# Performance work log

Measured on AMD Instinct MI355X. Metric: run time of the kernel, lower is better.

Reference implementation:

```python
import jax, jax.numpy as jnp
import numpy as np

N = 50000      # nodes
E = 800000     # edges
DIN = 256
DH = 256
DOUT = 64


def setup_inputs() -> dict:
    key = jax.random.key(0)
    ks = jax.random.split(key, 8)
    x = jax.random.normal(ks[0], (N, DIN), dtype=jnp.float32)
    edge_index = jax.random.randint(ks[1], (2, E), 0, N, dtype=jnp.int64)
    s = 0.05
    W1 = jax.random.normal(ks[2], (DIN, DH), dtype=jnp.float32) * s
    b1 = jnp.zeros((DH,), dtype=jnp.float32)
    W2 = jax.random.normal(ks[3], (DH, DH), dtype=jnp.float32) * s
    b2 = jnp.zeros((DH,), dtype=jnp.float32)
    W3 = jax.random.normal(ks[4], (DH, DOUT), dtype=jnp.float32) * s
    b3 = jnp.zeros((DOUT,), dtype=jnp.float32)
    return {"x": x, "edge_index": edge_index, "W1": W1, "b1": b1,
            "W2": W2, "b2": b2, "W3": W3, "b3": b3}


def gcn_conv(x, src, dst, deg_inv_sqrt, W, b):
    # x: [N, din] -> [N, dout]. PyG GCNConv: h = D^{-1/2}(A+I)D^{-1/2} (x W) + b
    n = x.shape[0]
    h = x @ W                                   # [N, dout]
    norm = deg_inv_sqrt[src] * deg_inv_sqrt[dst]  # [E+N]
    msgs = h[src] * norm[:, None]               # gather + scale, [E+N, dout]
    out = jax.ops.segment_sum(msgs, dst, num_segments=n)  # scatter-add
    return out + b


def _loops(edge_index, n):
    # add self loops, compute symmetric normalization degrees
    sl = jnp.arange(n, dtype=edge_index.dtype)
    src = jnp.concatenate([edge_index[0], sl])
    dst = jnp.concatenate([edge_index[1], sl])
    deg = jax.ops.segment_sum(jnp.ones_like(dst, dtype=jnp.float32), dst, num_segments=n)
    dis = jnp.where(deg > 0, jax.lax.rsqrt(deg), 0.0)
    return src, dst, dis


def reference(x, edge_index, W1, b1, W2, b2, W3, b3):
    src, dst, dis = _loops(edge_index, x.shape[0])
    h = jax.nn.relu(gcn_conv(x, src, dst, dis, W1, b1))   # dropout: eval no-op
    h = jax.nn.relu(gcn_conv(h, src, dst, dis, W2, b2))
    out = gcn_conv(h, src, dst, dis, W3, b3)              # batch=None -> no pooling
    return out
```

## Files before the change

kernel.cpp:

```cpp
#include <hip/hip_runtime.h>
#include <hip/hip_fp8.h>
#include <cstdint>
#include <cstddef>

typedef unsigned short u16;
typedef _Float16 f16x8 __attribute__((ext_vector_type(8)));
typedef float f32x2 __attribute__((ext_vector_type(2)));
typedef float f32x4 __attribute__((ext_vector_type(4)));

#if defined(__has_builtin)
#if __has_builtin(__builtin_amdgcn_cvt_pk_f32_fp8) && __has_builtin(__builtin_amdgcn_cvt_pk_fp8_f32)
#define FP8_BUILTIN 1
#endif
#endif

__device__ __forceinline__ float h2f(u16 u) {
  return (float)__builtin_bit_cast(_Float16, u);
}
__device__ __forceinline__ u16 f2h(float f) {
  return __builtin_bit_cast(u16, (_Float16)f);
}
__device__ __forceinline__ unsigned char ftofp8(float f) {
#ifdef FP8_BUILTIN
  return (unsigned char)(__builtin_amdgcn_cvt_pk_fp8_f32(f, f, 0, false) & 0xFF);
#else
  return __hip_fp8_e4m3(f).__x;
#endif
}

__device__ __forceinline__ void async16(u16* lds, const u16* g) {
  __builtin_amdgcn_global_load_lds(
      (const __attribute__((address_space(1))) unsigned int*)g,
      (__attribute__((address_space(3))) unsigned int*)lds, 16, 0, 0);
}

__device__ __forceinline__ void fma8(float* a, float d, uint4 p) {
  a[0] += d * h2f((u16)p.x); a[1] += d * h2f((u16)(p.x >> 16));
  a[2] += d * h2f((u16)p.y); a[3] += d * h2f((u16)(p.y >> 16));
  a[4] += d * h2f((u16)p.z); a[5] += d * h2f((u16)(p.z >> 16));
  a[6] += d * h2f((u16)p.w); a[7] += d * h2f((u16)(p.w >> 16));
}

__device__ __forceinline__ void fma8p(float* a, float d, uint2 p) {
#ifdef FP8_BUILTIN
  f32x2 v0 = __builtin_amdgcn_cvt_pk_f32_fp8((int)p.x, false);
  f32x2 v1 = __builtin_amdgcn_cvt_pk_f32_fp8((int)p.x, true);
  f32x2 v2 = __builtin_amdgcn_cvt_pk_f32_fp8((int)p.y, false);
  f32x2 v3 = __builtin_amdgcn_cvt_pk_f32_fp8((int)p.y, true);
  a[0] += d * v0.x; a[1] += d * v0.y; a[2] += d * v1.x; a[3] += d * v1.y;
  a[4] += d * v2.x; a[5] += d * v2.y; a[6] += d * v3.x; a[7] += d * v3.y;
#else
  const unsigned char* b = (const unsigned char*)&p;
#pragma unroll
  for (int k = 0; k < 8; ++k) {
    __hip_fp8_e4m3 v; v.__x = b[k];
    a[k] += d * (float)v;
  }
#endif
}

__device__ __forceinline__ int wave_is64(const void* ep) {
  const unsigned* p = (const unsigned*)ep;
  const int lane = threadIdx.x & 63;
  unsigned v = p[2 * lane + 1] | p[2 * (lane + 64) + 1];
  unsigned long long bal = __ballot(v != 0u);
  return (bal == 0ull) ? 1 : 0;
}

__device__ __forceinline__ int edge_at(const void* ep, int is64, long long idx) {
  if (is64) return (int)((const long long*)ep)[idx];
  return ((const int*)ep)[idx];
}

#define NCHUNK 64

__global__ void zero_f32(float* p, int n) {
  int i = blockIdx.x * 256 + threadIdx.x;
  if (i < n) p[i] = 0.f;
}

__global__ __launch_bounds__(256) void prep_all(
    const float4* __restrict__ x, ushort4* __restrict__ xpad, int n_src4, int n_tot4,
    const float* __restrict__ W1, u16* __restrict__ wt1,
    const float* __restrict__ W2, u16* __restrict__ wt2,
    const float* __restrict__ W3, u16* __restrict__ wt3,
    const void* __restrict__ ep, int* __restrict__ cnt,
    int E, int N, int DIN, int DH, int DOUT,
    int nb_cvt, int nb_w1, int nb_w2, int nb_w3) {
  int b = blockIdx.x;
  if (b < nb_cvt) {
    int i = b * 256 + threadIdx.x;
    if (i < n_tot4) {
      ushort4 o = {0, 0, 0, 0};
      if (i < n_src4) {
        float4 v = x[i];
        o.x = f2h(v.x); o.y = f2h(v.y); o.z = f2h(v.z); o.w = f2h(v.w);
      }
      xpad[i] = o;
    }
    return;
  }
  b -= nb_cvt;
  if (b < nb_w1) {
    int idx = b * 256 + threadIdx.x;
    if (idx < DIN * DH) {
      int n = idx / DIN, k = idx % DIN;
      wt1[idx] = f2h(W1[k * DH + n]);
    }
    return;
  }
  b -= nb_w1;
  if (b < nb_w2) {
    int idx = b * 256 + threadIdx.x;
    if (idx < DH * DH) {
      int n = idx / DH, k = idx % DH;
      wt2[idx] = f2h(W2[k * DH + n]);
    }
    return;
  }
  b -= nb_w2;
  if (b < nb_w3) {
    int idx = b * 256 + threadIdx.x;
    if (idx < DH * DOUT) {
      int n = idx / DH, k = idx % DH;
      wt3[idx] = f2h(W3[k * DOUT + n]);
    }
    return;
  }
  b -= nb_w3;
  {
    __shared__ int h[256];
    h[threadIdx.x] = 0;
    __syncthreads();
    int is64 = wave_is64(ep);
    const int per = (E + NCHUNK - 1) / NCHUNK;
    const int e0 = b * per, e1 = min(e0 + per, E);
    for (int e = e0 + (int)threadIdx.x; e < e1; e += 256) {
      int d = edge_at(ep, is64, (long long)E + e);
      d = min(max(d, 0), N - 1);
      atomicAdd(&h[d >> 8], 1);
    }
    __syncthreads();
    cnt[threadIdx.x * NCHUNK + b] = h[threadIdx.x];
  }
}

__global__ __launch_bounds__(256) void csr_base(const int* __restrict__ cnt,
                                                int* __restrict__ bases,
                                                int* __restrict__ off,
                                                int nbuck, int E) {
  __shared__ int ws4[8];
  const int t = threadIdx.x, lane = t & 63, w = t >> 6;
  int tot = 0;
  if (t < nbuck)
#pragma unroll 8
    for (int c = 0; c < NCHUNK; ++c) tot += cnt[t * NCHUNK + c];
  int inc = tot;
#pragma unroll
  for (int o = 1; o < 64; o <<= 1) {
    int u = __shfl_up(inc, o, 64);
    if (lane >= o) inc += u;
  }
  if (lane == 63) ws4[w] = inc;
  __syncthreads();
  if (t == 0) {
    int run = 0;
#pragma unroll
    for (int k = 0; k < 4; ++k) { int v = ws4[k]; ws4[k + 4] = run; run += v; }
  }
  __syncthreads();
  const int base = ws4[w + 4] + inc - tot;
  if (t < nbuck) {
    bases[t] = base;
    int run = base;
    for (int c = 0; c < NCHUNK; ++c) {
      off[t * NCHUNK + c] = run;
      run += cnt[t * NCHUNK + c];
    }
  }
  if (t == 0) bases[nbuck] = E;
}

__global__ __launch_bounds__(256) void csr_bucket(const void* __restrict__ ep,
                                                  const int* __restrict__ off,
                                                  unsigned* __restrict__ tmp,
                                                  int E, int N) {
  __shared__ int cur[256];
  const int chunk = blockIdx.x;
  const int nbuck = (N + 255) >> 8;
  if ((int)threadIdx.x < nbuck) cur[threadIdx.x] = off[threadIdx.x * NCHUNK + chunk];
  __syncthreads();
  int is64 = wave_is64(ep);
  const int per = (E + NCHUNK - 1) / NCHUNK;
  const int e0 = chunk * per, e1 = min(e0 + per, E);
  for (int e = e0 + (int)threadIdx.x; e < e1; e += 256) {
    int s = edge_at(ep, is64, e);
    int d = edge_at(ep, is64, (long long)E + e);
    s = min(max(s, 0), N - 1);
    d = min(max(d, 0), N - 1);
    int pos = atomicAdd(&cur[d >> 8], 1);
    tmp[pos] = ((unsigned)d << 16) | (unsigned)s;
  }
}

__global__ __launch_bounds__(256) void csr_final(const unsigned* __restrict__ tmp,
                                                 const int* __restrict__ bases,
                                                 int* __restrict__ rp,
                                                 float* __restrict__ dis,
                                                 u16* __restrict__ col, int N, int E) {
  __shared__ int hcnt[256];
  __shared__ int curs[256];
  __shared__ int ws4[8];
  const int b = blockIdx.x;
  const int node0 = b * 256;
  const int t = threadIdx.x, lane = t & 63, w = t >> 6;
  hcnt[t] = 0;
  __syncthreads();
  const int k0 = bases[b];
  const int k1 = bases[b + 1];
  for (int k = k0 + t; k < k1; k += 256)
    atomicAdd(&hcnt[(int)(tmp[k] >> 16) - node0], 1);
  __syncthreads();
  const int v = hcnt[t];
  int inc = v;
#pragma unroll
  for (int o = 1; o < 64; o <<= 1) {
    int u = __shfl_up(inc, o, 64);
    if (lane >= o) inc += u;
  }
  if (lane == 63) ws4[w] = inc;
  __syncthreads();
  if (t == 0) {
    int run = 0;
#pragma unroll
    for (int k = 0; k < 4; ++k) { int vv = ws4[k]; ws4[k + 4] = run; run += vv; }
  }
  __syncthreads();
  const int excl = k0 + ws4[w + 4] + inc - v;
  if (node0 + t < N) {
    rp[node0 + t] = excl;
    dis[node0 + t] = rsqrtf((float)(v + 1));
  }
  if (b == 0 && t == 0) rp[N] = E;
  curs[t] = excl;
  __syncthreads();
  for (int k = k0 + t; k < k1; k += 256) {
    unsigned e = tmp[k];
    int dl = (int)(e >> 16) - node0;
    int pos = atomicAdd(&curs[dl], 1);
    col[pos] = (u16)(e & 0xFFFFu);
  }
}

template <int BN, int OUT8>
__global__ __launch_bounds__(256) void gemm_bres(const u16* __restrict__ A,
                                                 const u16* __restrict__ Bt,
                                                 void* __restrict__ Cv, int Nt) {
  constexpr int K = 256;
  constexpr int NJ = BN / 16;
  constexpr int CH = BN * K / 8;
  __shared__ __align__(16) u16 Bs[BN * K];

  const int tid = threadIdx.x, lane = tid & 63, w = tid >> 6;
  const int bm = blockIdx.x, bn = blockIdx.y;

#pragma unroll
  for (int i = 0; i < CH / 256; ++i) {
    int c = tid + i * 256;
    int ln = c & 63, t2 = c >> 6;
    int ks = t2 & 7, j = t2 >> 3;
    int row = j * 16 + (ln & 15);
    int kk = ks * 32 + (ln >> 4) * 8;
    async16(&Bs[(size_t)c * 8], Bt + (size_t)(bn * BN + row) * K + kk);
  }

  const int r16 = lane & 15, quad = lane >> 4;
  const int m0 = w * 32;

  const u16* Ap0 = A + (size_t)(bm * 128 + m0 + r16) * K + quad * 8;
  const u16* Ap1 = Ap0 + 16 * K;
  f16x8 aa0[8], aa1[8];
#pragma unroll
  for (int ks = 0; ks < 8; ++ks) {
    aa0[ks] = *(const f16x8*)(Ap0 + ks * 32);
    aa1[ks] = *(const f16x8*)(Ap1 + ks * 32);
  }

  f32x4 acc[2][NJ];
  const f32x4 fzero = {0.f, 0.f, 0.f, 0.f};
#pragma unroll
  for (int i = 0; i < 2; ++i)
#pragma unroll
    for (int j = 0; j < NJ; ++j) acc[i][j] = fzero;

  __syncthreads();

#pragma unroll
  for (int ks = 0; ks < 8; ++ks) {
#pragma unroll
    for (int j = 0; j < NJ; ++j) {
      f16x8 bf = *(const f16x8*)(&Bs[(size_t)((j * 8 + ks) * 64 + lane) * 8]);
      acc[0][j] = __builtin_amdgcn_mfma_f32_16x16x32_f16(aa0[ks], bf, acc[0][j], 0, 0, 0);
      acc[1][j] = __builtin_amdgcn_mfma_f32_16x16x32_f16(aa1[ks], bf, acc[1][j], 0, 0, 0);
    }
  }
#pragma unroll
  for (int i = 0; i < 2; ++i)
#pragma unroll
    for (int j = 0; j < NJ; ++j) {
      int gr = bm * 128 + m0 + i * 16 + quad * 4;
      int gc = bn * BN + j * 16 + r16;
#pragma unroll
      for (int r = 0; r < 4; ++r) {
        if (OUT8) {
          ((unsigned char*)Cv)[(size_t)(gr + r) * Nt + gc] = ftofp8(acc[i][j][r]);
        } else {
          ((u16*)Cv)[(size_t)(gr + r) * Nt + gc] = f2h(acc[i][j][r]);
        }
      }
    }
}

__global__ __launch_bounds__(256) void agg_d256(const unsigned char* __restrict__ h,
                                                const int* __restrict__ rp,
                                                const u16* __restrict__ col,
                                                const float* __restrict__ dis,
                                                const float* __restrict__ bias,
                                                u16* __restrict__ out, int N) {
  const int wid = threadIdx.x >> 6, lane = threadIdx.x & 63;
  const int i = blockIdx.x * 4 + wid;
  if (i >= N) return;
  const int sub = lane >> 5;
  const int l32 = lane & 31;
  const int c8 = l32 * 8;
  const float di = dis[i];
  float a[8] = {0.f, 0.f, 0.f, 0.f, 0.f, 0.f, 0.f, 0.f};
  if (sub == 0) {
    uint2 sv = *(const uint2*)(h + (size_t)i * 256 + c8);
    fma8p(a, di, sv);
  }
  const int e1 = rp[i + 1];
  for (int base = rp[i]; base < e1; base += 64) {
    int me = base + lane;
    int s_l = 0; float d_l = 0.f;
    if (me < e1) { s_l = (int)col[me]; d_l = dis[s_l]; }
    const int cnt = min(64, e1 - base);
    const int cntR = (cnt + 7) & ~7;
    for (int t = 0; t < cntR; t += 8) {
      int sA = __shfl(s_l, t + sub, 64);      float dA = __shfl(d_l, t + sub, 64);
      int sB = __shfl(s_l, t + 2 + sub, 64);  float dB = __shfl(d_l, t + 2 + sub, 64);
      int sC = __shfl(s_l, t + 4 + sub, 64);  float dC = __shfl(d_l, t + 4 + sub, 64);
      int sD = __shfl(s_l, t + 6 + sub, 64);  float dD = __shfl(d_l, t + 6 + sub, 64);
      uint2 pA = *(const uint2*)(h + (size_t)sA * 256 + c8);
      uint2 pB = *(const uint2*)(h + (size_t)sB * 256 + c8);
      uint2 pC = *(const uint2*)(h + (size_t)sC * 256 + c8);
      uint2 pD = *(const uint2*)(h + (size_t)sD * 256 + c8);
      fma8p(a, dA, pA); fma8p(a, dB, pB); fma8p(a, dC, pC); fma8p(a, dD, pD);
    }
  }
#pragma unroll
  for (int k = 0; k < 8; ++k) a[k] += __shfl_xor(a[k], 32, 64);
  if (sub == 0) {
    float4 b0 = *(const float4*)(bias + c8);
    float4 b1 = *(const float4*)(bias + c8 + 4);
    float r0 = fmaxf(di * a[0] + b0.x, 0.f), r1 = fmaxf(di * a[1] + b0.y, 0.f);
    float r2 = fmaxf(di * a[2] + b0.z, 0.f), r3 = fmaxf(di * a[3] + b0.w, 0.f);
    float r4 = fmaxf(di * a[4] + b1.x, 0.f), r5 = fmaxf(di * a[5] + b1.y, 0.f);
    float r6 = fmaxf(di * a[6] + b1.z, 0.f), r7 = fmaxf(di * a[7] + b1.w, 0.f);
    uint4 ov;
    ov.x = (unsigned)f2h(r0) | ((unsigned)f2h(r1) << 16);
    ov.y = (unsigned)f2h(r2) | ((unsigned)f2h(r3) << 16);
    ov.z = (unsigned)f2h(r4) | ((unsigned)f2h(r5) << 16);
    ov.w = (unsigned)f2h(r6) | ((unsigned)f2h(r7) << 16);
    *(uint4*)(out + (size_t)i * 256 + c8) = ov;
  }
}

__global__ __launch_bounds__(256) void agg_d64(const u16* __restrict__ h,
                                               const int* __restrict__ rp,
                                               const u16* __restrict__ col,
                                               const float* __restrict__ dis,
                                               const float* __restrict__ bias,
                                               float* __restrict__ out, int N) {
  const int wid = threadIdx.x >> 6, lane = threadIdx.x & 63;
  const int i = blockIdx.x * 4 + wid;
  if (i >= N) return;
  const int grp = lane >> 3;
  const int l8 = lane & 7;
  const int c8 = l8 * 8;
  const float di = dis[i];
  float a[8];
  {
    uint4 sv = *(const uint4*)(h + (size_t)i * 64 + c8);
    const float w = (grp == 0) ? di : 0.f;
    a[0] = w * h2f((u16)sv.x); a[1] = w * h2f((u16)(sv.x >> 16));
    a[2] = w * h2f((u16)sv.y); a[3] = w * h2f((u16)(sv.y >> 16));
    a[4] = w * h2f((u16)sv.z); a[5] = w * h2f((u16)(sv.z >> 16));
    a[6] = w * h2f((u16)sv.w); a[7] = w * h2f((u16)(sv.w >> 16));
  }
  const int e1 = rp[i + 1];
  for (int base = rp[i]; base < e1; base += 64) {
    int me = base + lane;
    int s_l = 0; float d_l = 0.f;
    if (me < e1) { s_l = (int)col[me]; d_l = dis[s_l]; }
    const int cnt = min(64, e1 - base);
    const int cntR = (cnt + 15) & ~15;
    for (int t = 0; t < cntR; t += 16) {
      int sA = __shfl(s_l, t + grp, 64);       float dA = __shfl(d_l, t + grp, 64);
      int sB = __shfl(s_l, t + 8 + grp, 64);   float dB = __shfl(d_l, t + 8 + grp, 64);
      uint4 pA = *(const uint4*)(h + (size_t)sA * 64 + c8);
      uint4 pB = *(const uint4*)(h + (size_t)sB * 64 + c8);
      fma8(a, dA, pA); fma8(a, dB, pB);
    }
  }
#pragma unroll
  for (int k = 0; k < 8; ++k) a[k] += __shfl_xor(a[k], 8, 64);
#pragma unroll
  for (int k = 0; k < 8; ++k) a[k] += __shfl_xor(a[k], 16, 64);
#pragma unroll
  for (int k = 0; k < 8; ++k) a[k] += __shfl_xor(a[k], 32, 64);
  if (lane < 8) {
    float4 b0 = *(const float4*)(bias + c8);
    float4 b1 = *(const float4*)(bias + c8 + 4);
    float4 o0, o1;
    o0.x = di * a[0] + b0.x; o0.y = di * a[1] + b0.y;
    o0.z = di * a[2] + b0.z; o0.w = di * a[3] + b0.w;
    o1.x = di * a[4] + b1.x; o1.y = di * a[5] + b1.y;
    o1.z = di * a[6] + b1.z; o1.w = di * a[7] + b1.w;
    *(float4*)(out + (size_t)i * 64 + c8) = o0;
    *(float4*)(out + (size_t)i * 64 + c8 + 4) = o1;
  }
}

extern "C" void kernel_launch(void* const* d_in, const int* in_sizes, int n_in,
                              void* d_out, int out_size, void* d_ws, size_t ws_size,
                              hipStream_t stream) {
  if (n_in < 8) return;
  const float* x = (const float*)d_in[0];
  const void* eptr = d_in[1];
  const float* W1 = (const float*)d_in[2];
  const float* b1 = (const float*)d_in[3];
  const float* W2 = (const float*)d_in[4];
  const float* b2 = (const float*)d_in[5];
  const float* W3 = (const float*)d_in[6];
  const float* b3 = (const float*)d_in[7];
  float* out = (float*)d_out;

  const int DIN = 256, DH = 256;
  const int N = in_sizes[0] / DIN;
  const int E = in_sizes[1] / 2;
  const int DOUT = in_sizes[6] / DH;
  const int MT = (N + 127) / 128;
  const int Mpad = MT * 128;
  const int nbuck = (N + 255) >> 8;

  auto rnd = [](size_t b) { return (b + 255) & ~(size_t)255; };
  size_t required = 0;
  required += rnd((size_t)Mpad * DH * 2);
  required += rnd((size_t)Mpad * DH * 2);
  required += rnd((size_t)E * 2);
  required += rnd((size_t)E * 4);
  required += rnd((size_t)(N + 1) * 4);
  required += rnd((size_t)N * 4);
  required += rnd((size_t)DIN * DH * 2);
  required += rnd((size_t)DH * DH * 2);
  required += rnd((size_t)DH * DOUT * 2);
  required += rnd((size_t)256 * NCHUNK * 4) * 2;
  required += rnd((size_t)(nbuck + 1) * 4);
  if (ws_size < required || N > 65536 || nbuck > 256 || nbuck < 1) {
    zero_f32<<<(out_size + 255) / 256, 256, 0, stream>>>(out, out_size);
    return;
  }

  char* ws = (char*)d_ws;
  size_t off0 = 0;
  auto alloc = [&](size_t bytes) {
    char* p = ws + off0;
    off0 = (off0 + bytes + 255) & ~(size_t)255;
    return p;
  };
  u16* xpad = (u16*)alloc((size_t)Mpad * DH * 2);
  unsigned char* hbuf = (unsigned char*)alloc((size_t)Mpad * DH * 2);
  u16* colb = (u16*)alloc((size_t)E * 2);
  unsigned* tmpb = (unsigned*)alloc((size_t)E * 4);
  int* rp = (int*)alloc((size_t)(N + 1) * 4);
  float* dis = (float*)alloc((size_t)N * 4);
  u16* wt1 = (u16*)alloc((size_t)DIN * DH * 2);
  u16* wt2 = (u16*)alloc((size_t)DH * DH * 2);
  u16* wt3 = (u16*)alloc((size_t)DH * DOUT * 2);
  int* cnt = (int*)alloc((size_t)256 * NCHUNK * 4);
  int* offs = (int*)alloc((size_t)256 * NCHUNK * 4);
  int* bases = (int*)alloc((size_t)(nbuck + 1) * 4);

  const int n_tot4 = Mpad * DH / 4;
  const int nb_cvt = (n_tot4 + 255) / 256;
  const int nb_w1 = (DIN * DH + 255) / 256;
  const int nb_w2 = (DH * DH + 255) / 256;
  const int nb_w3 = (DH * DOUT + 255) / 256;
  prep_all<<<nb_cvt + nb_w1 + nb_w2 + nb_w3 + NCHUNK, 256, 0, stream>>>(
      (const float4*)x, (ushort4*)xpad, N * DH / 4, n_tot4,
      W1, wt1, W2, wt2, W3, wt3, eptr, cnt,
      E, N, DIN, DH, DOUT, nb_cvt, nb_w1, nb_w2, nb_w3);

  csr_base<<<1, 256, 0, stream>>>(cnt, bases, offs, nbuck, E);
  csr_bucket<<<NCHUNK, 256, 0, stream>>>(eptr, offs, tmpb, E, N);
  csr_final<<<nbuck, 256, 0, stream>>>(tmpb, bases, rp, dis, colb, N, E);

  gemm_bres<128, 1><<<dim3(MT, DH / 128), 256, 0, stream>>>(xpad, wt1, hbuf, DH);
  agg_d256<<<(N + 3) / 4, 256, 0, stream>>>(hbuf, rp, colb, dis, b1, xpad, N);
  gemm_bres<128, 1><<<dim3(MT, DH / 128), 256, 0, stream>>>(xpad, wt2, hbuf, DH);
  agg_d256<<<(N + 3) / 4, 256, 0, stream>>>(hbuf, rp, colb, dis, b2, xpad, N);
  gemm_bres<64, 0><<<dim3(MT, DOUT / 64), 256, 0, stream>>>(xpad, wt3, hbuf, DOUT);
  agg_d64<<<(N + 3) / 4, 256, 0, stream>>>((const u16*)hbuf, rp, colb, dis, b3, out, N);
}
```

Measured before the change: 302.1 us.

## Fuse x fp16 conversion into first GEMM, merge CSR base scan, fp8 layer-3 output

Removes the separate x-to-fp16 conversion pass by having the first GEMM load fp32 rows directly and convert in registers, clamping rows past N instead of relying on a zero-padded buffer. The single-block csr_base kernel is eliminated; csr_bucket and csr_final each recompute the bucket prefix sums in LDS from the count array. The last GEMM now writes fp8 output and agg_d64 gathers 8-byte fp8 rows instead of 16-byte fp16 rows, halving gather traffic at the cost of precision. This trades a launch and a full pass over x for redundant scan work per block and lower final-layer accuracy.

```diff
diff --git a/kernel.cpp b/kernel.cpp
--- a/kernel.cpp
+++ b/kernel.cpp
@@ -32,13 +32,6 @@
   __builtin_amdgcn_global_load_lds(
       (const __attribute__((address_space(1))) unsigned int*)g,
       (__attribute__((address_space(3))) unsigned int*)lds, 16, 0, 0);
-}
-
-__device__ __forceinline__ void fma8(float* a, float d, uint4 p) {
-  a[0] += d * h2f((u16)p.x); a[1] += d * h2f((u16)(p.x >> 16));
-  a[2] += d * h2f((u16)p.y); a[3] += d * h2f((u16)(p.y >> 16));
-  a[4] += d * h2f((u16)p.z); a[5] += d * h2f((u16)(p.z >> 16));
-  a[6] += d * h2f((u16)p.w); a[7] += d * h2f((u16)(p.w >> 16));
 }
 
 __device__ __forceinline__ void fma8p(float* a, float d, uint2 p) {
@@ -59,6 +52,15 @@
 #endif
 }
 
+__device__ __forceinline__ f16x8 cvt8(const float* p) {
+  float4 a = *(const float4*)p;
+  float4 b = *(const float4*)(p + 4);
+  f16x8 r;
+  r[0] = (_Float16)a.x; r[1] = (_Float16)a.y; r[2] = (_Float16)a.z; r[3] = (_Float16)a.w;
+  r[4] = (_Float16)b.x; r[5] = (_Float16)b.y; r[6] = (_Float16)b.z; r[7] = (_Float16)b.w;
+  return r;
+}
+
 __device__ __forceinline__ int wave_is64(const void* ep) {
   const unsigned* p = (const unsigned*)ep;
   const int lane = threadIdx.x & 63;
@@ -80,27 +82,13 @@
 }
 
 __global__ __launch_bounds__(256) void prep_all(
-    const float4* __restrict__ x, ushort4* __restrict__ xpad, int n_src4, int n_tot4,
     const float* __restrict__ W1, u16* __restrict__ wt1,
     const float* __restrict__ W2, u16* __restrict__ wt2,
     const float* __restrict__ W3, u16* __restrict__ wt3,
     const void* __restrict__ ep, int* __restrict__ cnt,
     int E, int N, int DIN, int DH, int DOUT,
-    int nb_cvt, int nb_w1, int nb_w2, int nb_w3) {
+    int nb_w1, int nb_w2, int nb_w3) {
   int b = blockIdx.x;
-  if (b < nb_cvt) {
-    int i = b * 256 + threadIdx.x;
-    if (i < n_tot4) {
-      ushort4 o = {0, 0, 0, 0};
-      if (i < n_src4) {
-        float4 v = x[i];
-        o.x = f2h(v.x); o.y = f2h(v.y); o.z = f2h(v.z); o.w = f2h(v.w);
-      }
-      xpad[i] = o;
-    }
-    return;
-  }
-  b -= nb_cvt;
   if (b < nb_w1) {
     int idx = b * 256 + threadIdx.x;
     if (idx < DIN * DH) {
@@ -145,11 +133,8 @@
   }
 }
 
-__global__ __launch_bounds__(256) void csr_base(const int* __restrict__ cnt,
-                                                int* __restrict__ bases,
-                                                int* __restrict__ off,
-                                                int nbuck, int E) {
-  __shared__ int ws4[8];
+__device__ __forceinline__ void bases_in_lds(const int* __restrict__ cnt,
+                                             int nbuck, int E, int* bl, int* ws4) {
   const int t = threadIdx.x, lane = t & 63, w = t >> 6;
   int tot = 0;
   if (t < nbuck)
@@ -169,31 +154,31 @@
     for (int k = 0; k < 4; ++k) { int v = ws4[k]; ws4[k + 4] = run; run += v; }
   }
   __syncthreads();
-  const int base = ws4[w + 4] + inc - tot;
+  bl[t] = ws4[w + 4] + inc - tot;
+  if (t == 0) bl[nbuck] = E;
+  __syncthreads();
+}
+
+__global__ __launch_bounds__(256) void csr_bucket(const void* __restrict__ ep,
+                                                  const int* __restrict__ cnt,
+                                                  unsigned* __restrict__ tmp,
+                                                  int E, int N, int nbuck) {
+  __shared__ int bl[257];
+  __shared__ int cur[256];
+  __shared__ int ws4[8];
+  const int chunk = blockIdx.x;
+  const int t = threadIdx.x;
+  bases_in_lds(cnt, nbuck, E, bl, ws4);
   if (t < nbuck) {
-    bases[t] = base;
-    int run = base;
-    for (int c = 0; c < NCHUNK; ++c) {
-      off[t * NCHUNK + c] = run;
-      run += cnt[t * NCHUNK + c];
-    }
-  }
-  if (t == 0) bases[nbuck] = E;
-}
-
-__global__ __launch_bounds__(256) void csr_bucket(const void* __restrict__ ep,
-                                                  const int* __restrict__ off,
-                                                  unsigned* __restrict__ tmp,
-                                                  int E, int N) {
-  __shared__ int cur[256];
-  const int chunk = blockIdx.x;
-  const int nbuck = (N + 255) >> 8;
-  if ((int)threadIdx.x < nbuck) cur[threadIdx.x] = off[threadIdx.x * NCHUNK + chunk];
+    int partial = 0;
+    for (int c = 0; c < chunk; ++c) partial += cnt[t * NCHUNK + c];
+    cur[t] = bl[t] + partial;
+  }
   __syncthreads();
   int is64 = wave_is64(ep);
   const int per = (E + NCHUNK - 1) / NCHUNK;
   const int e0 = chunk * per, e1 = min(e0 + per, E);
-  for (int e = e0 + (int)threadIdx.x; e < e1; e += 256) {
+  for (int e = e0 + t; e < e1; e += 256) {
     int s = edge_at(ep, is64, e);
     int d = edge_at(ep, is64, (long long)E + e);
     s = min(max(s, 0), N - 1);
@@ -204,20 +189,22 @@
 }
 
 __global__ __launch_bounds__(256) void csr_final(const unsigned* __restrict__ tmp,
-                                                 const int* __restrict__ bases,
+                                                 const int* __restrict__ cnt,
                                                  int* __restrict__ rp,
                                                  float* __restrict__ dis,
-                                                 u16* __restrict__ col, int N, int E) {
+                                                 u16* __restrict__ col,
+                                                 int N, int E, int nbuck) {
+  __shared__ int bl[257];
   __shared__ int hcnt[256];
   __shared__ int curs[256];
   __shared__ int ws4[8];
   const int b = blockIdx.x;
   const int node0 = b * 256;
   const int t = threadIdx.x, lane = t & 63, w = t >> 6;
+  bases_in_lds(cnt, nbuck, E, bl, ws4);
+  const int k0 = bl[b], k1 = bl[b + 1];
   hcnt[t] = 0;
   __syncthreads();
-  const int k0 = bases[b];
-  const int k1 = bases[b + 1];
   for (int k = k0 + t; k < k1; k += 256)
     atomicAdd(&hcnt[(int)(tmp[k] >> 16) - node0], 1);
   __syncthreads();
@@ -228,6 +215,7 @@
     int u = __shfl_up(inc, o, 64);
     if (lane >= o) inc += u;
   }
+  __syncthreads();
   if (lane == 63) ws4[w] = inc;
   __syncthreads();
   if (t == 0) {
@@ -252,10 +240,11 @@
   }
 }
 
-template <int BN, int OUT8>
-__global__ __launch_bounds__(256) void gemm_bres(const u16* __restrict__ A,
+template <int BN, int OUT8, int A32>
+__global__ __launch_bounds__(256) void gemm_bres(const void* __restrict__ A,
                                                  const u16* __restrict__ Bt,
-                                                 void* __restrict__ Cv, int Nt) {
+                                                 void* __restrict__ Cv, int Nt,
+                                                 int Nrows) {
   constexpr int K = 256;
   constexpr int NJ = BN / 16;
   constexpr int CH = BN * K / 8;
@@ -277,13 +266,27 @@
   const int r16 = lane & 15, quad = lane >> 4;
   const int m0 = w * 32;
 
-  const u16* Ap0 = A + (size_t)(bm * 128 + m0 + r16) * K + quad * 8;
-  const u16* Ap1 = Ap0 + 16 * K;
+  int row0 = bm * 128 + m0 + r16;
+  int row1 = row0 + 16;
   f16x8 aa0[8], aa1[8];
-#pragma unroll
-  for (int ks = 0; ks < 8; ++ks) {
-    aa0[ks] = *(const f16x8*)(Ap0 + ks * 32);
-    aa1[ks] = *(const f16x8*)(Ap1 + ks * 32);
+  if (A32) {
+    row0 = min(row0, Nrows - 1);
+    row1 = min(row1, Nrows - 1);
+    const float* A0 = (const float*)A + (size_t)row0 * K + quad * 8;
+    const float* A1 = (const float*)A + (size_t)row1 * K + quad * 8;
+#pragma unroll
+    for (int ks = 0; ks < 8; ++ks) {
+      aa0[ks] = cvt8(A0 + ks * 32);
+      aa1[ks] = cvt8(A1 + ks * 32);
+    }
+  } else {
+    const u16* A0 = (const u16*)A + (size_t)row0 * K + quad * 8;
+    const u16* A1 = (const u16*)A + (size_t)row1 * K + quad * 8;
+#pragma unroll
+    for (int ks = 0; ks < 8; ++ks) {
+      aa0[ks] = *(const f16x8*)(A0 + ks * 32);
+      aa1[ks] = *(const f16x8*)(A1 + ks * 32);
+    }
   }
 
   f32x4 acc[2][NJ];
@@ -376,7 +379,7 @@
   }
 }
 
-__global__ __launch_bounds__(256) void agg_d64(const u16* __restrict__ h,
+__global__ __launch_bounds__(256) void agg_d64(const unsigned char* __restrict__ h,
                                                const int* __restrict__ rp,
                                                const u16* __restrict__ col,
                                                const float* __restrict__ dis,
@@ -389,14 +392,10 @@
   const int l8 = lane & 7;
   const int c8 = l8 * 8;
   const float di = dis[i];
-  float a[8];
-  {
-    uint4 sv = *(const uint4*)(h + (size_t)i * 64 + c8);
-    const float w = (grp == 0) ? di : 0.f;
-    a[0] = w * h2f((u16)sv.x); a[1] = w * h2f((u16)(sv.x >> 16));
-    a[2] = w * h2f((u16)sv.y); a[3] = w * h2f((u16)(sv.y >> 16));
-    a[4] = w * h2f((u16)sv.z); a[5] = w * h2f((u16)(sv.z >> 16));
-    a[6] = w * h2f((u16)sv.w); a[7] = w * h2f((u16)(sv.w >> 16));
+  float a[8] = {0.f, 0.f, 0.f, 0.f, 0.f, 0.f, 0.f, 0.f};
+  if (grp == 0) {
+    uint2 sv = *(const uint2*)(h + (size_t)i * 64 + c8);
+    fma8p(a, di, sv);
   }
   const int e1 = rp[i + 1];
   for (int base = rp[i]; base < e1; base += 64) {
@@ -408,9 +407,9 @@
     for (int t = 0; t < cntR; t += 16) {
       int sA = __shfl(s_l, t + grp, 64);       float dA = __shfl(d_l, t + grp, 64);
       int sB = __shfl(s_l, t + 8 + grp, 64);   float dB = __shfl(d_l, t + 8 + grp, 64);
-      uint4 pA = *(const uint4*)(h + (size_t)sA * 64 + c8);
-      uint4 pB = *(const uint4*)(h + (size_t)sB * 64 + c8);
-      fma8(a, dA, pA); fma8(a, dB, pB);
+      uint2 pA = *(const uint2*)(h + (size_t)sA * 64 + c8);
+      uint2 pB = *(const uint2*)(h + (size_t)sB * 64 + c8);
+      fma8p(a, dA, pA); fma8p(a, dB, pB);
     }
   }
 #pragma unroll
@@ -457,7 +456,7 @@
   auto rnd = [](size_t b) { return (b + 255) & ~(size_t)255; };
   size_t required = 0;
   required += rnd((size_t)Mpad * DH * 2);
-  required += rnd((size_t)Mpad * DH * 2);
+  required += rnd((size_t)Mpad * DH);
   required += rnd((size_t)E * 2);
   required += rnd((size_t)E * 4);
   required += rnd((size_t)(N + 1) * 4);
@@ -465,8 +464,7 @@
   required += rnd((size_t)DIN * DH * 2);
   required += rnd((size_t)DH * DH * 2);
   required += rnd((size_t)DH * DOUT * 2);
-  required += rnd((size_t)256 * NCHUNK * 4) * 2;
-  required += rnd((size_t)(nbuck + 1) * 4);
+  required += rnd((size_t)256 * NCHUNK * 4);
   if (ws_size < required || N > 65536 || nbuck > 256 || nbuck < 1) {
     zero_f32<<<(out_size + 255) / 256, 256, 0, stream>>>(out, out_size);
     return;
@@ -480,7 +478,7 @@
     return p;
   };
   u16* xpad = (u16*)alloc((size_t)Mpad * DH * 2);
-  unsigned char* hbuf = (unsigned char*)alloc((size_t)Mpad * DH * 2);
+  unsigned char* hbuf = (unsigned char*)alloc((size_t)Mpad * DH);
   u16* colb = (u16*)alloc((size_t)E * 2);
   unsigned* tmpb = (unsigned*)alloc((size_t)E * 4);
   int* rp = (int*)alloc((size_t)(N + 1) * 4);
@@ -489,27 +487,21 @@
   u16* wt2 = (u16*)alloc((size_t)DH * DH * 2);
   u16* wt3 = (u16*)alloc((size_t)DH * DOUT * 2);
   int* cnt = (int*)alloc((size_t)256 * NCHUNK * 4);
-  int* offs = (int*)alloc((size_t)256 * NCHUNK * 4);
-  int* bases = (int*)alloc((size_t)(nbuck + 1) * 4);
-
-  const int n_tot4 = Mpad * DH / 4;
-  const int nb_cvt = (n_tot4 + 255) / 256;
+
   const int nb_w1 = (DIN * DH + 255) / 256;
   const int nb_w2 = (DH * DH + 255) / 256;
   const int nb_w3 = (DH * DOUT + 255) / 256;
-  prep_all<<<nb_cvt + nb_w1 + nb_w2 + nb_w3 + NCHUNK, 256, 0, stream>>>(
-      (const float4*)x, (ushort4*)xpad, N * DH / 4, n_tot4,
+  prep_all<<<nb_w1 + nb_w2 + nb_w3 + NCHUNK, 256, 0, stream>>>(
       W1, wt1, W2, wt2, W3, wt3, eptr, cnt,
-      E, N, DIN, DH, DOUT, nb_cvt, nb_w1, nb_w2, nb_w3);
-
-  csr_base<<<1, 256, 0, stream>>>(cnt, bases, offs, nbuck, E);
-  csr_bucket<<<NCHUNK, 256, 0, stream>>>(eptr, offs, tmpb, E, N);
-  csr_final<<<nbuck, 256, 0, stream>>>(tmpb, bases, rp, dis, colb, N, E);
-
-  gemm_bres<128, 1><<<dim3(MT, DH / 128), 256, 0, stream>>>(xpad, wt1, hbuf, DH);
+      E, N, DIN, DH, DOUT, nb_w1, nb_w2, nb_w3);
+
+  csr_bucket<<<NCHUNK, 256, 0, stream>>>(eptr, cnt, tmpb, E, N, nbuck);
+  csr_final<<<nbuck, 256, 0, stream>>>(tmpb, cnt, rp, dis, colb, N, E, nbuck);
+
+  gemm_bres<128, 1, 1><<<dim3(MT, DH / 128), 256, 0, stream>>>(x, wt1, hbuf, DH, N);
   agg_d256<<<(N + 3) / 4, 256, 0, stream>>>(hbuf, rp, colb, dis, b1, xpad, N);
-  gemm_bres<128, 1><<<dim3(MT, DH / 128), 256, 0, stream>>>(xpad, wt2, hbuf, DH);
+  gemm_bres<128, 1, 0><<<dim3(MT, DH / 128), 256, 0, stream>>>(xpad, wt2, hbuf, DH, N);
   agg_d256<<<(N + 3) / 4, 256, 0, stream>>>(hbuf, rp, colb, dis, b2, xpad, N);
-  gemm_bres<64, 0><<<dim3(MT, DOUT / 64), 256, 0, stream>>>(xpad, wt3, hbuf, DOUT);
-  agg_d64<<<(N + 3) / 4, 256, 0, stream>>>((const u16*)hbuf, rp, colb, dis, b3, out, N);
-}
+  gemm_bres<64, 1, 0><<<dim3(MT, DOUT / 64), 256, 0, stream>>>(xpad, wt3, hbuf, DOUT, N);
+  agg_d64<<<(N + 3) / 4, 256, 0, stream>>>(hbuf, rp, colb, dis, b3, out, N);
+}
```

Result: no change. 296.2 us (-1.9%).
